# Optimization experiments

Measured on AMD Instinct MI355X. Metric: run time of the kernel, lower is better.

## Reference

```python
import jax, jax.numpy as jnp
import numpy as np

S, B, C, H, E = 4096, 2, 256, 8, 131072
CC = C // H


def setup_inputs() -> dict:
    key = jax.random.key(0)
    ks = jax.random.split(key, 12)
    sc = 0.02
    inp = {
        "x": jax.random.normal(ks[0], (S, B, C), jnp.float32),
        "q_id": jax.random.randint(ks[1], (E,), 0, S, jnp.int32),
        "k_id": jax.random.randint(ks[2], (E,), 0, S, jnp.int32),
        "Wq": jax.random.normal(ks[3], (C, C), jnp.float32) * sc,
        "bq": jnp.zeros((C,), jnp.float32),
        "Wk": jax.random.normal(ks[4], (C, C), jnp.float32) * sc,
        "bk": jnp.zeros((C,), jnp.float32),
        "Wv": jax.random.normal(ks[5], (C, C), jnp.float32) * sc,
        "bv": jnp.zeros((C,), jnp.float32),
        "Wx": jax.random.normal(ks[6], (C, C), jnp.float32) * sc,
        "bx": jnp.zeros((C,), jnp.float32),
    }
    return inp


def reference(x, q_id, k_id, Wq, bq, Wk, bk, Wv, bv, Wx, bx):
    s, b, c = x.shape
    cc = c // H
    # qkv projections (torch Linear: x @ W.T + b)
    q = (x @ Wq.T + bq).reshape(s, b, H, cc)
    k = (x @ Wk.T + bk).reshape(s, b, H, cc)
    v = (x @ Wv.T + bv).reshape(s, b, H, cc)
    # per-edge scores: gather along sequence axis by edge ids
    qk = jnp.einsum('ebhc,ebhc->ebh', q[q_id], k[k_id])[..., None]  # [E,b,h,1]
    qk = qk / jnp.sqrt(jnp.asarray(cc, x.dtype))
    eqk = jnp.exp(qk - jnp.max(qk))  # global max, as in original
    # scatter-add softmax normalizer and weighted sum over edges
    d = jnp.zeros((s, b, H, 1), x.dtype).at[q_id].add(eqk)
    out = jnp.zeros((s, b, H, cc), x.dtype).at[q_id].add(eqk * v[k_id])
    out = (out / d).reshape(s, b, c)
    return out @ Wx.T + bx
```

## Files before the change

### kernel.cpp

```cpp
#include <hip/hip_runtime.h>

constexpr int S_  = 4096;
constexpr int B_  = 2;
constexpr int C_  = 256;
constexpr int H_  = 8;
constexpr int E_  = 131072;
constexpr int CC_ = 32;
constexpr int MR  = S_ * B_;

typedef __attribute__((ext_vector_type(8))) short bf16x8_t;
typedef __attribute__((ext_vector_type(4))) float f32x4_t;

__device__ __forceinline__ unsigned short f2bf(float f) {
    unsigned int u = __float_as_uint(f);
    u += 0x7fffu + ((u >> 16) & 1u);
    return (unsigned short)(u >> 16);
}
__device__ __forceinline__ float bflo(unsigned int u) { return __uint_as_float(u << 16); }
__device__ __forceinline__ float bfhi(unsigned int u) { return __uint_as_float(u & 0xffff0000u); }

__device__ __forceinline__ void cast8(const float* __restrict__ src, unsigned short* __restrict__ dst, int i) {
    const float4* s = (const float4*)src + (size_t)i * 2;
    float4 a = s[0], b = s[1];
    uint4 o;
    o.x = (unsigned)f2bf(a.x) | ((unsigned)f2bf(a.y) << 16);
    o.y = (unsigned)f2bf(a.z) | ((unsigned)f2bf(a.w) << 16);
    o.z = (unsigned)f2bf(b.x) | ((unsigned)f2bf(b.y) << 16);
    o.w = (unsigned)f2bf(b.z) | ((unsigned)f2bf(b.w) << 16);
    *((uint4*)dst + i) = o;
}


__global__ __launch_bounds__(256) void prep_kernel(
        const int* __restrict__ q_id, int* __restrict__ count,
        const float* __restrict__ x, unsigned short* __restrict__ xb,
        const float* __restrict__ Wq, const float* __restrict__ Wk,
        const float* __restrict__ Wv, const float* __restrict__ Wx,
        unsigned short* __restrict__ Wb) {
    const int bid = blockIdx.x, tid = threadIdx.x;
    if (bid < 512) {
        atomicAdd(&count[q_id[bid * 256 + tid]], 1);
    } else if (bid < 1536) {
        cast8(x, xb, (bid - 512) * 256 + tid);
    } else {
        int idx = bid - 1536;
        int z = idx >> 5;
        const float* src = (z == 0) ? Wq : (z == 1) ? Wk : (z == 2) ? Wv : Wx;
        cast8(src, Wb + (size_t)z * (C_ * C_), (idx & 31) * 256 + tid);
    }
}


__global__ __launch_bounds__(1024) void scan_kernel(const int* __restrict__ count,
                                                    int* __restrict__ base,
                                                    int* __restrict__ cursor) {
    __shared__ int wsums[16];
    const int t = threadIdx.x, lane = t & 63, w = t >> 6;
    int c0 = count[4 * t + 0], c1 = count[4 * t + 1];
    int c2 = count[4 * t + 2], c3 = count[4 * t + 3];
    int tsum = c0 + c1 + c2 + c3;
    int x = tsum;
#pragma unroll
    for (int off = 1; off < 64; off <<= 1) {
        int y = __shfl_up(x, off);
        if (lane >= off) x += y;
    }
    if (lane == 63) wsums[w] = x;
    __syncthreads();
    if (t == 0) {
        int run = 0;
#pragma unroll
        for (int i = 0; i < 16; ++i) { int v = wsums[i]; wsums[i] = run; run += v; }
        base[S_] = run;
    }
    __syncthreads();
    int excl = x - tsum + wsums[w];
    int b0 = excl, b1 = b0 + c0, b2 = b1 + c1, b3 = b2 + c2;
    base[4 * t + 0] = b0; base[4 * t + 1] = b1;
    base[4 * t + 2] = b2; base[4 * t + 3] = b3;
    cursor[4 * t + 0] = b0; cursor[4 * t + 1] = b1;
    cursor[4 * t + 2] = b2; cursor[4 * t + 3] = b3;
}


__global__ __launch_bounds__(256) void scatter_qkv_kernel(
        const int* __restrict__ q_id, const int* __restrict__ k_id,
        int* __restrict__ cursor, int* __restrict__ koff_sorted,
        const unsigned short* __restrict__ xb, const unsigned short* __restrict__ Wb,
        const float* __restrict__ bq, const float* __restrict__ bk, const float* __restrict__ bv,
        unsigned short* __restrict__ qb, unsigned short* __restrict__ kvb) {
    __shared__ __align__(16) unsigned short As[64][264];
    const int bid = blockIdx.x, tid = threadIdx.x;
    if (bid < 512) {
        int e = bid * 256 + tid;
        int pos = atomicAdd(&cursor[q_id[e]], 1);
        koff_sorted[pos] = k_id[e] << 10;
        return;
    }
    const int u = bid - 512;
    const int nb = u % 12, mg = u / 12;
    const int lane = tid & 63, wave = tid >> 6;
    const int l16 = lane & 15, quad = lane >> 4;
    const int z = nb >> 2;
    const int colz = ((nb & 3) << 6) + (wave << 4);

    const unsigned short* Wrow = Wb + (size_t)z * (C_ * C_) + (size_t)(colz + l16) * C_;
    bf16x8_t breg[8];
#pragma unroll
    for (int ks = 0; ks < 8; ++ks)
        breg[ks] = *(const bf16x8_t*)(Wrow + ks * 32 + quad * 8);

    const float* bias = (z == 0) ? bq : (z == 1) ? bk : bv;
    const float bcol = bias[colz + l16];
    unsigned short* ob = (z == 0) ? qb : kvb;
    const int ostr = (z == 0) ? 256 : 512;
    const int ocol = ((z == 2) ? 256 : 0) + colz + l16;

    const int c0 = (mg * 128) / 43, c1 = ((mg + 1) * 128) / 43;
    for (int c = c0; c < c1; ++c) {
        const int mbase = c * 64;
        __syncthreads();
#pragma unroll
        for (int it = 0; it < 8; ++it) {
            int l = it * 256 + tid;
            int r = l >> 5, cc = (l & 31) << 3;
            *(uint4*)&As[r][cc] = *(const uint4*)&xb[(size_t)(mbase + r) * C_ + cc];
        }
        __syncthreads();
#pragma unroll
        for (int mt = 0; mt < 4; ++mt) {
            f32x4_t acc = {0.f, 0.f, 0.f, 0.f};
#pragma unroll
            for (int ks = 0; ks < 8; ++ks) {
                bf16x8_t a = *(const bf16x8_t*)&As[mt * 16 + l16][ks * 32 + quad * 8];
                acc = __builtin_amdgcn_mfma_f32_16x16x32_bf16(a, breg[ks], acc, 0, 0, 0);
            }
            const int row0 = mbase + mt * 16 + quad * 4;
#pragma unroll
            for (int r = 0; r < 4; ++r)
                ob[(size_t)(row0 + r) * ostr + ocol] = f2bf(acc[r] + bcol);
        }
    }
}


__global__ __launch_bounds__(256) void attn_edge(
        const unsigned short* __restrict__ qb, const unsigned short* __restrict__ kvb,
        const int* __restrict__ base, const int* __restrict__ koff,
        unsigned short* __restrict__ attnb) {
    __shared__ float red[2][64][9];
    const int lane = threadIdx.x & 63;
    const int wave = threadIdx.x >> 6;
    const int rw = wave >> 1, part = wave & 1;
    const int s = blockIdx.x * 2 + rw;
    const int half = lane >> 5, hl = lane & 31;
    const int e0 = __builtin_amdgcn_readfirstlane(base[s]);
    const int e1 = __builtin_amdgcn_readfirstlane(base[s + 1]);

    const uint4 qq = *((const uint4*)(qb + (size_t)(s * 2 + half) * C_) + hl);
    const float q0 = bflo(qq.x), q1 = bfhi(qq.x), q2 = bflo(qq.y), q3 = bfhi(qq.y);
    const float q4 = bflo(qq.z), q5 = bfhi(qq.z), q6 = bflo(qq.w), q7 = bfhi(qq.w);

    float a0 = 0.f, a1 = 0.f, a2 = 0.f, a3 = 0.f, a4 = 0.f, a5 = 0.f, a6 = 0.f, a7 = 0.f;
    float wsum = 0.f;
    const float scale = 0.17677669529663687f;

    auto edge = [&](const uint4& kk, const uint4& vv) {
        float p = q0 * bflo(kk.x) + q1 * bfhi(kk.x)
                + q2 * bflo(kk.y) + q3 * bfhi(kk.y)
                + q4 * bflo(kk.z) + q5 * bfhi(kk.z)
                + q6 * bflo(kk.w) + q7 * bfhi(kk.w);
        p += __shfl_xor(p, 1);
        p += __shfl_xor(p, 2);
        const float w = __expf(p * scale);
        a0 = fmaf(w, bflo(vv.x), a0); a1 = fmaf(w, bfhi(vv.x), a1);
        a2 = fmaf(w, bflo(vv.y), a2); a3 = fmaf(w, bfhi(vv.y), a3);
        a4 = fmaf(w, bflo(vv.z), a4); a5 = fmaf(w, bfhi(vv.z), a5);
        a6 = fmaf(w, bflo(vv.w), a6); a7 = fmaf(w, bfhi(vv.w), a7);
        wsum += w;
    };
    auto fetch = [&](int my, int t, uint4& kk, uint4& vv) {
        int o = __builtin_amdgcn_readlane(my, part + 2 * t);
        const uint4* p = (const uint4*)(kvb + o + half * 512);
        kk = p[hl]; vv = p[32 + hl];
    };

    for (int b0 = e0; b0 < e1; b0 += 64) {
        const int m = min(64, e1 - b0);
        const int my = koff[b0 + ((lane < m) ? lane : 0)];
        const int nm = (m > part) ? ((m - part + 1) >> 1) : 0;
        uint4 kka = {}, vva = {}, kkb = {}, vvb = {};
        if (nm > 0) fetch(my, 0, kka, vva);
        if (nm > 1) fetch(my, 1, kkb, vvb);
        int t = 0;
        for (; t + 3 < nm; t += 2) {
            edge(kka, vva);
            fetch(my, t + 2, kka, vva);
            edge(kkb, vvb);
            fetch(my, t + 3, kkb, vvb);
        }
        if (t < nm)     edge(kka, vva);
        if (t + 1 < nm) edge(kkb, vvb);
        if (t + 2 < nm) { fetch(my, t + 2, kka, vva); edge(kka, vva); }
    }

    if (part == 1) {
        float* r = red[rw][lane];
        r[0] = a0; r[1] = a1; r[2] = a2; r[3] = a3;
        r[4] = a4; r[5] = a5; r[6] = a6; r[7] = a7; r[8] = wsum;
    }
    __syncthreads();
    if (part == 0) {
        const float* r = red[rw][lane];
        a0 += r[0]; a1 += r[1]; a2 += r[2]; a3 += r[3];
        a4 += r[4]; a5 += r[5]; a6 += r[6]; a7 += r[7]; wsum += r[8];
        const float inv = 1.0f / wsum;
        uint4 o;
        o.x = (unsigned)f2bf(a0 * inv) | ((unsigned)f2bf(a1 * inv) << 16);
        o.y = (unsigned)f2bf(a2 * inv) | ((unsigned)f2bf(a3 * inv) << 16);
        o.z = (unsigned)f2bf(a4 * inv) | ((unsigned)f2bf(a5 * inv) << 16);
        o.w = (unsigned)f2bf(a6 * inv) | ((unsigned)f2bf(a7 * inv) << 16);
        *((uint4*)(attnb + (size_t)(s * 2 + half) * C_) + hl) = o;
    }
}


__global__ __launch_bounds__(256) void gemm_proj(
        const unsigned short* __restrict__ attnb, const unsigned short* __restrict__ Wxb,
        const float* __restrict__ bx, float* __restrict__ out) {
    __shared__ __align__(16) unsigned short As[64][264];
    const int tid = threadIdx.x;
    const int nb = blockIdx.x & 3, mg = blockIdx.x >> 2;
    const int lane = tid & 63, wave = tid >> 6;
    const int l16 = lane & 15, quad = lane >> 4;
    const int colz = (nb << 6) + (wave << 4);

    const unsigned short* Wrow = Wxb + (size_t)(colz + l16) * C_;
    bf16x8_t breg[8];
#pragma unroll
    for (int ks = 0; ks < 8; ++ks)
        breg[ks] = *(const bf16x8_t*)(Wrow + ks * 32 + quad * 8);
    const float bcol = bx[colz + l16];
    const int ocol = colz + l16;

    const int mbase = mg * 64;
#pragma unroll
    for (int it = 0; it < 8; ++it) {
        int l = it * 256 + tid;
        int r = l >> 5, cc = (l & 31) << 3;
        *(uint4*)&As[r][cc] = *(const uint4*)&attnb[(size_t)(mbase + r) * C_ + cc];
    }
    __syncthreads();
#pragma unroll
    for (int mt = 0; mt < 4; ++mt) {
        f32x4_t acc = {0.f, 0.f, 0.f, 0.f};
#pragma unroll
        for (int ks = 0; ks < 8; ++ks) {
            bf16x8_t a = *(const bf16x8_t*)&As[mt * 16 + l16][ks * 32 + quad * 8];
            acc = __builtin_amdgcn_mfma_f32_16x16x32_bf16(a, breg[ks], acc, 0, 0, 0);
        }
        const int row0 = mbase + mt * 16 + quad * 4;
#pragma unroll
        for (int r = 0; r < 4; ++r)
            out[(size_t)(row0 + r) * C_ + ocol] = acc[r] + bcol;
    }
}


extern "C" void kernel_launch(void* const* d_in, const int* in_sizes, int n_in,
                              void* d_out, int out_size, void* d_ws, size_t ws_size,
                              hipStream_t stream) {
    const float* x  = (const float*)d_in[0];
    const int* q_id = (const int*)d_in[1];
    const int* k_id = (const int*)d_in[2];
    const float* Wq = (const float*)d_in[3];
    const float* bq = (const float*)d_in[4];
    const float* Wk = (const float*)d_in[5];
    const float* bk = (const float*)d_in[6];
    const float* Wv = (const float*)d_in[7];
    const float* bv = (const float*)d_in[8];
    const float* Wx = (const float*)d_in[9];
    const float* bx = (const float*)d_in[10];
    float* out = (float*)d_out;

    char* ws = (char*)d_ws;
    unsigned short* xb    = (unsigned short*)ws;                 ws += (size_t)MR * C_ * 2;
    unsigned short* qb    = (unsigned short*)ws;                 ws += (size_t)MR * C_ * 2;
    unsigned short* kvb   = (unsigned short*)ws;                 ws += (size_t)MR * 512 * 2;
    unsigned short* attnb = (unsigned short*)ws;                 ws += (size_t)MR * C_ * 2;
    unsigned short* Wb    = (unsigned short*)ws;                 ws += (size_t)4 * C_ * C_ * 2;
    int* count       = (int*)ws;                                 ws += S_ * 4;
    int* base        = (int*)ws;                                 ws += (S_ + 1) * 4;
    int* cursor      = (int*)ws;                                 ws += S_ * 4;
    int* koff_sorted = (int*)ws;

    hipMemsetAsync(count, 0, S_ * sizeof(int), stream);
    prep_kernel<<<1664, 256, 0, stream>>>(q_id, count, x, xb, Wq, Wk, Wv, Wx, Wb);
    scan_kernel<<<1, 1024, 0, stream>>>(count, base, cursor);
    scatter_qkv_kernel<<<1028, 256, 0, stream>>>(q_id, k_id, cursor, koff_sorted,
                                                 xb, Wb, bq, bk, bv, qb, kvb);
    attn_edge<<<S_ / 2, 256, 0, stream>>>(qb, kvb, base, koff_sorted, attnb);
    gemm_proj<<<512, 256, 0, stream>>>(attnb, Wb + (size_t)3 * C_ * C_, bx, out);
}
```

Before: 147.6 us.

## Fuse all stages into one cooperative persistent kernel with grid syncs

Replaces the five separate launches (prep, scan, scatter+QKV GEMM, edge attention, output projection) with one cooperative kernel of 512 blocks that separates the phases with grid-wide syncs. Each block loops over its share of the work units. The scan is rewritten for 256 threads handling 16 counts each, and the edge scatter now runs in its own phase after the QKV GEMM. The goal is to remove launch gaps and inter-kernel drain, at the cost of four grid barriers, lower parallelism in the attention phase (persistent blocks with an occupancy hint of 2), and a serial scan inside one block. If the cooperative launch fails, the code falls back to the separate kernels.

```diff
diff --git a/kernel.cpp b/kernel.cpp
--- a/kernel.cpp
+++ b/kernel.cpp
@@ -1,4 +1,7 @@
 #include <hip/hip_runtime.h>
+#include <hip/hip_cooperative_groups.h>
+
+namespace cg = cooperative_groups;
 
 constexpr int S_  = 4096;
 constexpr int B_  = 2;
@@ -31,35 +34,14 @@
 }
 
 
-__global__ __launch_bounds__(256) void prep_kernel(
-        const int* __restrict__ q_id, int* __restrict__ count,
-        const float* __restrict__ x, unsigned short* __restrict__ xb,
-        const float* __restrict__ Wq, const float* __restrict__ Wk,
-        const float* __restrict__ Wv, const float* __restrict__ Wx,
-        unsigned short* __restrict__ Wb) {
-    const int bid = blockIdx.x, tid = threadIdx.x;
-    if (bid < 512) {
-        atomicAdd(&count[q_id[bid * 256 + tid]], 1);
-    } else if (bid < 1536) {
-        cast8(x, xb, (bid - 512) * 256 + tid);
-    } else {
-        int idx = bid - 1536;
-        int z = idx >> 5;
-        const float* src = (z == 0) ? Wq : (z == 1) ? Wk : (z == 2) ? Wv : Wx;
-        cast8(src, Wb + (size_t)z * (C_ * C_), (idx & 31) * 256 + tid);
-    }
-}
-
-
-__global__ __launch_bounds__(1024) void scan_kernel(const int* __restrict__ count,
-                                                    int* __restrict__ base,
-                                                    int* __restrict__ cursor) {
-    __shared__ int wsums[16];
+__device__ __forceinline__ void scan_body(const int* __restrict__ count,
+                                          int* __restrict__ base, int* __restrict__ cursor,
+                                          int* wsums ) {
     const int t = threadIdx.x, lane = t & 63, w = t >> 6;
-    int c0 = count[4 * t + 0], c1 = count[4 * t + 1];
-    int c2 = count[4 * t + 2], c3 = count[4 * t + 3];
-    int tsum = c0 + c1 + c2 + c3;
-    int x = tsum;
+    int c[16]; int s = 0;
+#pragma unroll
+    for (int i = 0; i < 16; ++i) { c[i] = count[t * 16 + i]; s += c[i]; }
+    int x = s;
 #pragma unroll
     for (int off = 1; off < 64; off <<= 1) {
         int y = __shfl_up(x, off);
@@ -70,34 +52,23 @@
     if (t == 0) {
         int run = 0;
 #pragma unroll
-        for (int i = 0; i < 16; ++i) { int v = wsums[i]; wsums[i] = run; run += v; }
+        for (int i = 0; i < 4; ++i) { int v = wsums[i]; wsums[i] = run; run += v; }
         base[S_] = run;
     }
     __syncthreads();
-    int excl = x - tsum + wsums[w];
-    int b0 = excl, b1 = b0 + c0, b2 = b1 + c1, b3 = b2 + c2;
-    base[4 * t + 0] = b0; base[4 * t + 1] = b1;
-    base[4 * t + 2] = b2; base[4 * t + 3] = b3;
-    cursor[4 * t + 0] = b0; cursor[4 * t + 1] = b1;
-    cursor[4 * t + 2] = b2; cursor[4 * t + 3] = b3;
-}
-
-
-__global__ __launch_bounds__(256) void scatter_qkv_kernel(
-        const int* __restrict__ q_id, const int* __restrict__ k_id,
-        int* __restrict__ cursor, int* __restrict__ koff_sorted,
+    int run = x - s + wsums[w];
+#pragma unroll
+    for (int i = 0; i < 16; ++i) {
+        base[t * 16 + i] = run; cursor[t * 16 + i] = run; run += c[i];
+    }
+}
+
+__device__ __forceinline__ void qkv_unit(
+        int u, int tid,
         const unsigned short* __restrict__ xb, const unsigned short* __restrict__ Wb,
         const float* __restrict__ bq, const float* __restrict__ bk, const float* __restrict__ bv,
-        unsigned short* __restrict__ qb, unsigned short* __restrict__ kvb) {
-    __shared__ __align__(16) unsigned short As[64][264];
-    const int bid = blockIdx.x, tid = threadIdx.x;
-    if (bid < 512) {
-        int e = bid * 256 + tid;
-        int pos = atomicAdd(&cursor[q_id[e]], 1);
-        koff_sorted[pos] = k_id[e] << 10;
-        return;
-    }
-    const int u = bid - 512;
+        unsigned short* __restrict__ qb, unsigned short* __restrict__ kvb,
+        unsigned short (*As)[264]) {
     const int nb = u % 12, mg = u / 12;
     const int lane = tid & 63, wave = tid >> 6;
     const int l16 = lane & 15, quad = lane >> 4;
@@ -143,16 +114,14 @@
     }
 }
 
-
-__global__ __launch_bounds__(256) void attn_edge(
+__device__ __forceinline__ void attn_pair(
+        int rb, int tid,
         const unsigned short* __restrict__ qb, const unsigned short* __restrict__ kvb,
         const int* __restrict__ base, const int* __restrict__ koff,
-        unsigned short* __restrict__ attnb) {
-    __shared__ float red[2][64][9];
-    const int lane = threadIdx.x & 63;
-    const int wave = threadIdx.x >> 6;
+        unsigned short* __restrict__ attnb, float* redbuf ) {
+    const int lane = tid & 63, wave = tid >> 6;
     const int rw = wave >> 1, part = wave & 1;
-    const int s = blockIdx.x * 2 + rw;
+    const int s = rb * 2 + rw;
     const int half = lane >> 5, hl = lane & 31;
     const int e0 = __builtin_amdgcn_readfirstlane(base[s]);
     const int e1 = __builtin_amdgcn_readfirstlane(base[s + 1]);
@@ -204,14 +173,13 @@
         if (t + 2 < nm) { fetch(my, t + 2, kka, vva); edge(kka, vva); }
     }
 
+    float* r = redbuf + (size_t)(rw * 64 + lane) * 9;
     if (part == 1) {
-        float* r = red[rw][lane];
         r[0] = a0; r[1] = a1; r[2] = a2; r[3] = a3;
         r[4] = a4; r[5] = a5; r[6] = a6; r[7] = a7; r[8] = wsum;
     }
     __syncthreads();
     if (part == 0) {
-        const float* r = red[rw][lane];
         a0 += r[0]; a1 += r[1]; a2 += r[2]; a3 += r[3];
         a4 += r[4]; a5 += r[5]; a6 += r[6]; a7 += r[7]; wsum += r[8];
         const float inv = 1.0f / wsum;
@@ -224,13 +192,12 @@
     }
 }
 
-
-__global__ __launch_bounds__(256) void gemm_proj(
+__device__ __forceinline__ void proj_unit(
+        int u, int tid,
         const unsigned short* __restrict__ attnb, const unsigned short* __restrict__ Wxb,
-        const float* __restrict__ bx, float* __restrict__ out) {
-    __shared__ __align__(16) unsigned short As[64][264];
-    const int tid = threadIdx.x;
-    const int nb = blockIdx.x & 3, mg = blockIdx.x >> 2;
+        const float* __restrict__ bx, float* __restrict__ out,
+        unsigned short (*As)[264]) {
+    const int nb = u & 3, mg = u >> 2;
     const int lane = tid & 63, wave = tid >> 6;
     const int l16 = lane & 15, quad = lane >> 4;
     const int colz = (nb << 6) + (wave << 4);
@@ -264,6 +231,114 @@
         for (int r = 0; r < 4; ++r)
             out[(size_t)(row0 + r) * C_ + ocol] = acc[r] + bcol;
     }
+}
+
+
+__global__ __launch_bounds__(256, 2) void mega_kernel(
+        const float* __restrict__ x, const int* __restrict__ q_id, const int* __restrict__ k_id,
+        const float* __restrict__ Wq, const float* __restrict__ bq,
+        const float* __restrict__ Wk, const float* __restrict__ bk,
+        const float* __restrict__ Wv, const float* __restrict__ bv,
+        const float* __restrict__ Wx, const float* __restrict__ bx,
+        float* __restrict__ out,
+        unsigned short* __restrict__ xb, unsigned short* __restrict__ qb,
+        unsigned short* __restrict__ kvb, unsigned short* __restrict__ attnb,
+        unsigned short* __restrict__ Wb,
+        int* __restrict__ count, int* __restrict__ base, int* __restrict__ cursor,
+        int* __restrict__ koff) {
+    cg::grid_group grid = cg::this_grid();
+    __shared__ __align__(16) char smem[64 * 264 * 2];
+    const int bid = blockIdx.x, tid = threadIdx.x;
+    const int gid = bid * 256 + tid;
+
+    cast8(x, xb, gid);
+    cast8(x, xb, gid + 131072);
+    if (gid < 32768) {
+        int z = gid >> 13;
+        const float* src = (z == 0) ? Wq : (z == 1) ? Wk : (z == 2) ? Wv : Wx;
+        cast8(src, Wb + (size_t)z * (C_ * C_), gid & 8191);
+    }
+    atomicAdd(&count[q_id[gid]], 1);
+    grid.sync();
+
+    if (bid == 511) scan_body(count, base, cursor, (int*)smem);
+    for (int u = bid; u < 516; u += 512)
+        qkv_unit(u, tid, xb, Wb, bq, bk, bv, qb, kvb, (unsigned short(*)[264])smem);
+    grid.sync();
+
+    {
+        int pos = atomicAdd(&cursor[q_id[gid]], 1);
+        koff[pos] = k_id[gid] << 10;
+    }
+    grid.sync();
+
+    for (int rb = bid; rb < 2048; rb += 512) {
+        __syncthreads();
+        attn_pair(rb, tid, qb, kvb, base, koff, attnb, (float*)smem);
+    }
+    grid.sync();
+
+    proj_unit(bid, tid, attnb, Wb + (size_t)3 * (C_ * C_), bx, out,
+              (unsigned short(*)[264])smem);
+}
+
+
+__global__ __launch_bounds__(256) void fb_prep(
+        const int* __restrict__ q_id, int* __restrict__ count,
+        const float* __restrict__ x, unsigned short* __restrict__ xb,
+        const float* __restrict__ Wq, const float* __restrict__ Wk,
+        const float* __restrict__ Wv, const float* __restrict__ Wx,
+        unsigned short* __restrict__ Wb) {
+    const int bid = blockIdx.x, tid = threadIdx.x;
+    if (bid < 512) {
+        atomicAdd(&count[q_id[bid * 256 + tid]], 1);
+    } else if (bid < 1536) {
+        cast8(x, xb, (bid - 512) * 256 + tid);
+    } else {
+        int idx = bid - 1536;
+        int z = idx >> 5;
+        const float* src = (z == 0) ? Wq : (z == 1) ? Wk : (z == 2) ? Wv : Wx;
+        cast8(src, Wb + (size_t)z * (C_ * C_), (idx & 31) * 256 + tid);
+    }
+}
+
+__global__ __launch_bounds__(256) void fb_scan(const int* __restrict__ count,
+                                               int* __restrict__ base,
+                                               int* __restrict__ cursor) {
+    __shared__ int wsums[4];
+    scan_body(count, base, cursor, wsums);
+}
+
+__global__ __launch_bounds__(256) void fb_scatter_qkv(
+        const int* __restrict__ q_id, const int* __restrict__ k_id,
+        int* __restrict__ cursor, int* __restrict__ koff,
+        const unsigned short* __restrict__ xb, const unsigned short* __restrict__ Wb,
+        const float* __restrict__ bq, const float* __restrict__ bk, const float* __restrict__ bv,
+        unsigned short* __restrict__ qb, unsigned short* __restrict__ kvb) {
+    __shared__ __align__(16) unsigned short As[64][264];
+    const int bid = blockIdx.x, tid = threadIdx.x;
+    if (bid < 512) {
+        int e = bid * 256 + tid;
+        int pos = atomicAdd(&cursor[q_id[e]], 1);
+        koff[pos] = k_id[e] << 10;
+        return;
+    }
+    qkv_unit(bid - 512, tid, xb, Wb, bq, bk, bv, qb, kvb, As);
+}
+
+__global__ __launch_bounds__(256) void fb_attn(
+        const unsigned short* __restrict__ qb, const unsigned short* __restrict__ kvb,
+        const int* __restrict__ base, const int* __restrict__ koff,
+        unsigned short* __restrict__ attnb) {
+    __shared__ float red[2 * 64 * 9];
+    attn_pair(blockIdx.x, threadIdx.x, qb, kvb, base, koff, attnb, red);
+}
+
+__global__ __launch_bounds__(256) void fb_proj(
+        const unsigned short* __restrict__ attnb, const unsigned short* __restrict__ Wxb,
+        const float* __restrict__ bx, float* __restrict__ out) {
+    __shared__ __align__(16) unsigned short As[64][264];
+    proj_unit(blockIdx.x, threadIdx.x, attnb, Wxb, bx, out, As);
 }
 
 
@@ -284,21 +359,34 @@
     float* out = (float*)d_out;
 
     char* ws = (char*)d_ws;
-    unsigned short* xb    = (unsigned short*)ws;                 ws += (size_t)MR * C_ * 2;
-    unsigned short* qb    = (unsigned short*)ws;                 ws += (size_t)MR * C_ * 2;
-    unsigned short* kvb   = (unsigned short*)ws;                 ws += (size_t)MR * 512 * 2;
-    unsigned short* attnb = (unsigned short*)ws;                 ws += (size_t)MR * C_ * 2;
-    unsigned short* Wb    = (unsigned short*)ws;                 ws += (size_t)4 * C_ * C_ * 2;
-    int* count       = (int*)ws;                                 ws += S_ * 4;
-    int* base        = (int*)ws;                                 ws += (S_ + 1) * 4;
-    int* cursor      = (int*)ws;                                 ws += S_ * 4;
-    int* koff_sorted = (int*)ws;
+    unsigned short* xb    = (unsigned short*)ws;   ws += (size_t)MR * C_ * 2;
+    unsigned short* qb    = (unsigned short*)ws;   ws += (size_t)MR * C_ * 2;
+    unsigned short* kvb   = (unsigned short*)ws;   ws += (size_t)MR * 512 * 2;
+    unsigned short* attnb = (unsigned short*)ws;   ws += (size_t)MR * C_ * 2;
+    unsigned short* Wb    = (unsigned short*)ws;   ws += (size_t)4 * C_ * C_ * 2;
+    int* count  = (int*)ws;                        ws += S_ * 4;
+    int* base   = (int*)ws;                        ws += (S_ + 1) * 4;
+    int* cursor = (int*)ws;                        ws += S_ * 4;
+    int* koff   = (int*)ws;
 
     hipMemsetAsync(count, 0, S_ * sizeof(int), stream);
-    prep_kernel<<<1664, 256, 0, stream>>>(q_id, count, x, xb, Wq, Wk, Wv, Wx, Wb);
-    scan_kernel<<<1, 1024, 0, stream>>>(count, base, cursor);
-    scatter_qkv_kernel<<<1028, 256, 0, stream>>>(q_id, k_id, cursor, koff_sorted,
+
+    void* args[] = {
+        (void*)&x, (void*)&q_id, (void*)&k_id,
+        (void*)&Wq, (void*)&bq, (void*)&Wk, (void*)&bk,
+        (void*)&Wv, (void*)&bv, (void*)&Wx, (void*)&bx,
+        (void*)&out,
+        (void*)&xb, (void*)&qb, (void*)&kvb, (void*)&attnb, (void*)&Wb,
+        (void*)&count, (void*)&base, (void*)&cursor, (void*)&koff,
+    };
+    hipError_t err = hipLaunchCooperativeKernel((const void*)mega_kernel,
+                                                dim3(512), dim3(256), args, 0, stream);
+    if (err != hipSuccess) {
+        fb_prep<<<1664, 256, 0, stream>>>(q_id, count, x, xb, Wq, Wk, Wv, Wx, Wb);
+        fb_scan<<<1, 256, 0, stream>>>(count, base, cursor);
+        fb_scatter_qkv<<<1028, 256, 0, stream>>>(q_id, k_id, cursor, koff,
                                                  xb, Wb, bq, bk, bv, qb, kvb);
-    attn_edge<<<S_ / 2, 256, 0, stream>>>(qb, kvb, base, koff_sorted, attnb);
-    gemm_proj<<<512, 256, 0, stream>>>(attnb, Wb + (size_t)3 * C_ * C_, bx, out);
-}
+        fb_attn<<<2048, 256, 0, stream>>>(qb, kvb, base, koff, attnb);
+        fb_proj<<<512, 256, 0, stream>>>(attnb, Wb + (size_t)3 * C_ * C_, bx, out);
+    }
+}
```

Measured after the change: 399.4 us. +170.6%, slower.
